# Kernel tuning notes

Hardware: AMD Instinct MI355X
Metric: run time of the kernel (lower is better)

Reference implementation:

```python
import jax, jax.numpy as jnp
import numpy as np

H = 768
NH = 12
HD = H // NH  # 64


def setup_inputs() -> dict:
    key = jax.random.key(0)
    ks = jax.random.split(key, 10)
    s = 0.02
    return {
        "hidden_states": jax.random.normal(ks[0], (2, 2048, H), dtype=jnp.float32),
        "attention_mask": jnp.ones((2, 2048), dtype=jnp.int32),
        "wq": jax.random.normal(ks[1], (H, H), dtype=jnp.float32) * s,
        "bq": jnp.zeros((H,), dtype=jnp.float32),
        "wk": jax.random.normal(ks[2], (H, H), dtype=jnp.float32) * s,
        "bk": jnp.zeros((H,), dtype=jnp.float32),
        "wv": jax.random.normal(ks[3], (H, H), dtype=jnp.float32) * s,
        "bv": jnp.zeros((H,), dtype=jnp.float32),
        "wo": jax.random.normal(ks[4], (H, H), dtype=jnp.float32) * s,
        "bo": jnp.zeros((H,), dtype=jnp.float32),
    }


def reference(hidden_states, attention_mask, wq, bq, wk, bk, wv, bv, wo, bo):
    b, s, h = hidden_states.shape
    # torch Linear: x @ W.T + b
    def proj(w, bias):
        y = jnp.einsum("bsh,oh->bso", hidden_states, w) + bias
        return y.reshape(b, s, NH, HD).transpose(0, 2, 1, 3)  # [b, nh, s, hd]

    q = proj(wq, bq)
    k = proj(wk, bk)
    v = proj(wv, bv)

    scores = jnp.einsum("bhqd,bhkd->bhqk", q, k) / jnp.sqrt(jnp.float32(HD))
    mask = attention_mask[:, None, None, :]  # [b,1,1,s]
    scores = jnp.where(mask == 0, jnp.float32(-1e9), scores)
    probs = jax.nn.softmax(scores, axis=-1)
    # dropout is identity in eval mode
    ctx = jnp.einsum("bhqk,bhkd->bhqd", probs, v)
    ctx = ctx.transpose(0, 2, 1, 3).reshape(b, s, h)
    return jnp.einsum("bsh,oh->bso", ctx, wo) + bo
```

## Files before the change

kernel.cpp:

```cpp
#include <hip/hip_runtime.h>

#define NH   12
#define HD   64
#define H    768
#define B_   2
#define S_   2048
#define MTOT (B_*S_)
#define SPLK 2

typedef short bf16x8 __attribute__((ext_vector_type(8)));
typedef float f32x4  __attribute__((ext_vector_type(4)));
typedef float f32x16 __attribute__((ext_vector_type(16)));
typedef unsigned uint32x2 __attribute__((ext_vector_type(2)));

#define MFMA16(a,b,c) __builtin_amdgcn_mfma_f32_16x16x32_bf16((a),(b),(c),0,0,0)
#define MFMA32(a,b,c) __builtin_amdgcn_mfma_f32_32x32x16_bf16((a),(b),(c),0,0,0)
#define GLL16(g,l) __builtin_amdgcn_global_load_lds( \
    (const __attribute__((address_space(1))) void*)(g), \
    (__attribute__((address_space(3))) void*)(l), 16, 0, 0)
#define EXP2F(x) __builtin_amdgcn_exp2f(x)
#define SCHEDB() __builtin_amdgcn_sched_barrier(0)
#define SBAR()   __builtin_amdgcn_s_barrier()

#if __has_builtin(__builtin_amdgcn_permlane32_swap)
__device__ __forceinline__ uint32x2 plswap(unsigned a, unsigned b){
    return __builtin_amdgcn_permlane32_swap(a, b, false, false);
}
#else
__device__ __forceinline__ uint32x2 plswap(unsigned a, unsigned b){
    const int hi = (threadIdx.x & 63) >> 5;
    const unsigned pa = (unsigned)__shfl_xor((int)a, 32);
    const unsigned pb = (unsigned)__shfl_xor((int)b, 32);
    uint32x2 r;
    r.x = hi ? pb : a;
    r.y = hi ? b  : pa;
    return r;
}
#endif

__device__ __forceinline__ float cross32_max(float x){
    uint32x2 r = plswap(__float_as_uint(x), __float_as_uint(x));
    return fmaxf(__uint_as_float(r.x), __uint_as_float(r.y));
}
__device__ __forceinline__ float cross32_add(float x){
    uint32x2 r = plswap(__float_as_uint(x), __float_as_uint(x));
    return __uint_as_float(r.x) + __uint_as_float(r.y);
}

__device__ __forceinline__ unsigned short f2bf(float x){
    union { float f; unsigned u; } c; c.f = x;
    unsigned r = (c.u + 0x7FFFu + ((c.u >> 16) & 1u)) >> 16;
    return (unsigned short)r;
}

#define XB 3072
#define WB 576
__global__ __launch_bounds__(256) void prep(
    const float* __restrict__ hs,
    const float* __restrict__ wq, const float* __restrict__ wk,
    const float* __restrict__ wv, const float* __restrict__ wo,
    unsigned short* __restrict__ Xh, unsigned short* __restrict__ Wqkv,
    unsigned short* __restrict__ Wo_)
{
    const int bid = blockIdx.x;
    const float* src;
    unsigned short* dst;
    int ib;
    if (bid < XB){
        src = hs; dst = Xh; ib = bid;
    } else {
        const int w = (bid - XB) / WB;
        ib = (bid - XB) - w*WB;
        src = (w==0)?wq:(w==1)?wk:(w==2)?wv:wo;
        dst = (w < 3) ? (Wqkv + (size_t)w*768*H) : Wo_;
    }
    const size_t i = (size_t)ib*256 + threadIdx.x;
    const float4 v = ((const float4*)src)[i];
    ushort4 o;
    o.x = f2bf(v.x); o.y = f2bf(v.y); o.z = f2bf(v.z); o.w = f2bf(v.w);
    ((ushort4*)dst)[i] = o;
}

template<int MODE>
__global__ __launch_bounds__(256) void gemm_bf16(
    const unsigned short* __restrict__ A, const unsigned short* __restrict__ Bm,
    const float* __restrict__ b0, const float* __restrict__ b1,
    const float* __restrict__ b2,
    float* __restrict__ out,
    unsigned short* __restrict__ Qh, unsigned short* __restrict__ Kh,
    unsigned short* __restrict__ Vh)
{
    constexpr int NIT = H/32;

    __shared__ unsigned short As[2][64*32];
    __shared__ unsigned short Bs[2][128*32];
    const int tid = threadIdx.x, lane = tid & 63, wave = tid >> 6;
    const int m0 = blockIdx.x*64, n0 = blockIdx.y*128;
    const int wr = wave >> 1, wc = wave & 1;
    const int frow = lane & 15, foct = lane >> 4;
    const int arow = lane >> 2;
    const int achk = ((lane & 3) ^ (arow & 3)) * 8;
    const int fswz = (foct ^ (frow & 3)) * 8;

    auto STAGE = [&](int bufi, int kp){
        {
            const int r0 = wave*16;
            GLL16(A + (size_t)(m0 + r0 + arow)*H + kp + achk, &As[bufi][r0*32]);
        }
        #pragma unroll
        for (int i = 0; i < 2; ++i){
            const int r0 = (wave*2 + i)*16;
            GLL16(Bm + (size_t)(n0 + r0 + arow)*H + kp + achk, &Bs[bufi][r0*32]);
        }
    };

    STAGE(0, 0);
    STAGE(1, 32);

    f32x4 acc[2][4] = {};

    for (int it = 0; it < NIT; ++it){
        const int cur = it & 1;
        if (it + 1 < NIT) asm volatile("s_waitcnt vmcnt(3)");
        else              asm volatile("s_waitcnt vmcnt(0)");
        SCHEDB();
        SBAR();
        SCHEDB();

        bf16x8 af[2], bfv[4];
        #pragma unroll
        for (int i = 0; i < 2; ++i)
            af[i]  = *(const bf16x8*)&As[cur][(wr*32 + 16*i + frow)*32 + fswz];
        #pragma unroll
        for (int j = 0; j < 4; ++j)
            bfv[j] = *(const bf16x8*)&Bs[cur][(wc*64 + 16*j + frow)*32 + fswz];
        #pragma unroll
        for (int i = 0; i < 2; ++i)
            #pragma unroll
            for (int j = 0; j < 4; ++j)
                acc[i][j] = MFMA16(af[i], bfv[j], acc[i][j]);

        SCHEDB();
        SBAR();
        SCHEDB();
        if (it + 2 < NIT) STAGE(cur, (it + 2)*32);
    }

    if (MODE == 0){
        #pragma unroll
        for (int i = 0; i < 2; ++i){
            const int m = m0 + wr*32 + 16*i + 4*foct;
            #pragma unroll
            for (int j = 0; j < 4; ++j){
                const int n = n0 + wc*64 + 16*j + frow;
                const float bb = b0[n];
                #pragma unroll
                for (int r = 0; r < 4; ++r)
                    out[(size_t)(m + r)*H + n] = acc[i][j][r] + bb;
            }
        }
    } else {
        const int sect = n0 / 768;
        const float* bias = (sect==0) ? b0 : (sect==1) ? b1 : b2;
        const float qs = (sect==0) ? 0.125f*1.44269504f : 1.0f;
        unsigned short* Ph = (sect==0) ? Qh : Kh;
        #pragma unroll
        for (int i = 0; i < 2; ++i){
            const int m  = m0 + wr*32 + 16*i + 4*foct;
            const int bb = m >> 11, ss = m & (S_-1);
            #pragma unroll
            for (int j = 0; j < 4; ++j){
                const int nn = (n0 - sect*768) + wc*64 + 16*j + frow;
                const float bv_ = bias[nn];
                const int hh = nn >> 6, dd = nn & 63;
                unsigned short hi[4];
                #pragma unroll
                for (int r = 0; r < 4; ++r)
                    hi[r] = f2bf((acc[i][j][r] + bv_) * qs);
                if (sect < 2){
                    const size_t basep = ((size_t)(bb*NH + hh)*S_)*HD + dd;
                    #pragma unroll
                    for (int r = 0; r < 4; ++r)
                        Ph[basep + (size_t)(ss + r)*HD] = hi[r];
                } else {
                    const size_t a = ((size_t)(bb*NH + hh)*HD + dd)*S_ + ss;
                    ushort4 ph; ph.x=hi[0]; ph.y=hi[1]; ph.z=hi[2]; ph.w=hi[3];
                    *(ushort4*)&Vh[a] = ph;
                }
            }
        }
    }
}

__global__ __launch_bounds__(256, 3) void attn_mfma(
    const unsigned short* __restrict__ Qh, const unsigned short* __restrict__ Kh,
    const unsigned short* __restrict__ Vh,
    const int* __restrict__ mask, float* __restrict__ Op, float* __restrict__ mlb)
{
    __shared__ unsigned short Ksh[2][64*64];
    __shared__ unsigned short Vsh[2][64*64];

    const int tid = threadIdx.x, lane = tid & 63, wave = tid >> 6;
    const int q0 = blockIdx.x*128, h = blockIdx.y;
    const int b = blockIdx.z & 1, part = blockIdx.z >> 1;
    const int l31 = lane & 31, hi = lane >> 5, l7 = lane & 7;
    const size_t base  = (size_t)(b*NH + h)*S_;
    const size_t vbase = (size_t)(b*NH + h)*HD;
    const int srow = lane >> 3;
    const int schk = ((lane & 7) ^ srow) * 8;
    const int NTH = 16;
    const int t0 = part*NTH;

    auto STAGE = [&](int bufi, int t){
        if (wave < 2){
            #pragma unroll
            for (int i = 0; i < 4; ++i){
                const int r0 = (wave*4 + i)*8, row = r0 + srow;
                GLL16(Kh + (base + (size_t)t*64 + row)*HD + schk, &Ksh[bufi][r0*64]);
            }
        } else {
            #pragma unroll
            for (int i = 0; i < 4; ++i){
                const int r0 = ((wave-2)*4 + i)*8, row = r0 + srow;
                GLL16(Vh + (vbase + row)*S_ + (size_t)t*64 + schk, &Vsh[bufi][r0*64]);
            }
        }
    };

    unsigned mbits = 0;
    {
        const int* mp = mask + (size_t)b*S_ + lane*32;
        #pragma unroll
        for (int j = 0; j < 32; ++j) mbits |= (mp[j] ? 1u : 0u) << j;
    }

    bf16x8 qf[4];
    {
        const size_t qr = (base + q0 + wave*32 + l31)*HD;
        #pragma unroll
        for (int ds = 0; ds < 4; ++ds)
            qf[ds] = *(const bf16x8*)&Qh[qr + ds*16 + hi*8];
    }

    STAGE(0, t0);
    STAGE(1, t0 + 1);

    float mR = -1e30f, lR = 0.f;
    f32x16 o0 = {}, o1 = {};

    for (int tt = 0; tt < NTH; ++tt){
        const int t = t0 + tt, cur = tt & 1;
        if (tt + 1 < NTH) asm volatile("s_waitcnt vmcnt(4)");
        else              asm volatile("s_waitcnt vmcnt(0)");
        SCHEDB();
        SBAR();
        SCHEDB();

        f32x16 s0 = {}, s1 = {};
        __builtin_amdgcn_s_setprio(1);
        #pragma unroll
        for (int ds = 0; ds < 4; ++ds){
            const int c0 = ((2*ds + hi) ^ l7)*8;
            const bf16x8 kh0 = *(const bf16x8*)&Ksh[cur][l31*64 + c0];
            const bf16x8 kh1 = *(const bf16x8*)&Ksh[cur][(32+l31)*64 + c0];
            s0 = MFMA32(kh0, qf[ds], s0);
            s1 = MFMA32(kh1, qf[ds], s1);
        }
        __builtin_amdgcn_s_setprio(0);

        {
            const unsigned bm_lo = (unsigned)__shfl((int)mbits, 2*t);
            const unsigned bm_hi = (unsigned)__shfl((int)mbits, 2*t + 1);
            const unsigned long long mb = ((unsigned long long)bm_hi << 32) | bm_lo;
            if (~mb){
                #pragma unroll
                for (int r = 0; r < 16; ++r){
                    const int key = (r&3) + 8*(r>>2) + 4*hi;
                    if (!((mb >> key) & 1))      s0[r] = -1e9f;
                    if (!((mb >> (key+32)) & 1)) s1[r] = -1e9f;
                }
            }
        }

        float vmax = -1e30f;
        #pragma unroll
        for (int r = 0; r < 16; ++r) vmax = fmaxf(vmax, fmaxf(s0[r], s1[r]));
        vmax = cross32_max(vmax);
        if (!__all(vmax <= mR + 11.5f)){
            const float mnew = fmaxf(mR, vmax);
            const float sc = EXP2F(mR - mnew);
            mR = mnew; lR *= sc;
            #pragma unroll
            for (int r = 0; r < 16; ++r){ o0[r] *= sc; o1[r] *= sc; }
        }
        float ps = 0.f;
        #pragma unroll
        for (int r = 0; r < 16; ++r){
            s0[r] = EXP2F(s0[r] - mR);
            s1[r] = EXP2F(s1[r] - mR);
            ps += s0[r] + s1[r];
        }
        ps = cross32_add(ps);
        lR += ps;

        bf16x8 pf[4];
        #pragma unroll
        for (int s = 0; s < 4; ++s){
            const f32x16& pv = (s < 2) ? s0 : s1;
            const int rb = (s & 1)*8;
            unsigned w0, w1, w2, w3;
            asm("v_cvt_pk_bf16_f32 %0, %1, %2" : "=v"(w0) : "v"(pv[rb+0]), "v"(pv[rb+1]));
            asm("v_cvt_pk_bf16_f32 %0, %1, %2" : "=v"(w1) : "v"(pv[rb+2]), "v"(pv[rb+3]));
            asm("v_cvt_pk_bf16_f32 %0, %1, %2" : "=v"(w2) : "v"(pv[rb+4]), "v"(pv[rb+5]));
            asm("v_cvt_pk_bf16_f32 %0, %1, %2" : "=v"(w3) : "v"(pv[rb+6]), "v"(pv[rb+7]));
            const uint32x2 r02 = plswap(w0, w2);
            const uint32x2 r13 = plswap(w1, w3);
            union { uint4 u; bf16x8 v; } pk;
            pk.u.x = r02.x; pk.u.y = r13.x; pk.u.z = r02.y; pk.u.w = r13.y;
            pf[s] = pk.v;
        }

        __builtin_amdgcn_s_setprio(1);
        #pragma unroll
        for (int s = 0; s < 4; ++s){
            const int c0 = ((2*s + hi) ^ l7)*8;
            const bf16x8 vh0 = *(const bf16x8*)&Vsh[cur][l31*64 + c0];
            const bf16x8 vh1 = *(const bf16x8*)&Vsh[cur][(32+l31)*64 + c0];
            o0 = MFMA32(vh0, pf[s], o0);
            o1 = MFMA32(vh1, pf[s], o1);
        }
        __builtin_amdgcn_s_setprio(0);

        SCHEDB();
        SBAR();
        SCHEDB();
        if (tt + 2 < NTH) STAGE(cur, t + 2);
    }

    const int qg = q0 + wave*32 + l31;
    const size_t NQ = (size_t)B_*NH*S_;
    const size_t gq = ((size_t)b*NH + h)*S_ + qg;
    float* Od = Op + (part*NQ + gq)*HD;
    #pragma unroll
    for (int a = 0; a < 4; ++a){
        const int d0 = 8*a + 4*hi;
        f32x4 v0, v1;
        #pragma unroll
        for (int r = 0; r < 4; ++r){ v0[r] = o0[a*4+r]; v1[r] = o1[a*4+r]; }
        *(f32x4*)&Od[d0]      = v0;
        *(f32x4*)&Od[32 + d0] = v1;
    }
    if (hi == 0){
        mlb[(part*NQ + gq)*2]     = mR;
        mlb[(part*NQ + gq)*2 + 1] = lR;
    }
}

__global__ __launch_bounds__(256) void attn_combine(
    const float* __restrict__ Op, const float* __restrict__ mlb,
    unsigned short* __restrict__ Cs)
{
    const int tid = threadIdx.x;
    const int gq = blockIdx.x*16 + (tid >> 4);
    const int dl = (tid & 15)*4;
    const int s = gq & (S_-1);
    const int bh = gq >> 11;
    const int h = bh % NH, b = bh / NH;
    const size_t NQ = (size_t)B_*NH*S_;

    float m_[SPLK], l_[SPLK];
    #pragma unroll
    for (int i = 0; i < SPLK; ++i){
        m_[i] = mlb[(i*NQ + gq)*2];
        l_[i] = mlb[(i*NQ + gq)*2 + 1];
    }
    float mm = m_[0];
    #pragma unroll
    for (int i = 1; i < SPLK; ++i) mm = fmaxf(mm, m_[i]);
    float w_[SPLK], den = 0.f;
    #pragma unroll
    for (int i = 0; i < SPLK; ++i){
        w_[i] = __builtin_amdgcn_exp2f(m_[i] - mm);
        den += l_[i]*w_[i];
    }
    const float inv = 1.0f / den;

    float v0 = 0.f, v1 = 0.f, v2 = 0.f, v3 = 0.f;
    #pragma unroll
    for (int i = 0; i < SPLK; ++i){
        const float4 O = *(const float4*)&Op[(i*NQ + gq)*HD + dl];
        v0 += O.x*w_[i]; v1 += O.y*w_[i]; v2 += O.z*w_[i]; v3 += O.w*w_[i];
    }
    v0 *= inv; v1 *= inv; v2 *= inv; v3 *= inv;

    ushort4 ph;
    ph.x = f2bf(v0); ph.y = f2bf(v1); ph.z = f2bf(v2); ph.w = f2bf(v3);
    *(ushort4*)&Cs[((size_t)b*S_ + s)*H + h*HD + dl] = ph;
}

extern "C" void kernel_launch(void* const* d_in, const int* in_sizes, int n_in,
                              void* d_out, int out_size, void* d_ws, size_t ws_size,
                              hipStream_t stream) {
    const float* hs = (const float*)d_in[0];
    const int*  msk = (const int*)  d_in[1];
    const float* wq = (const float*)d_in[2];
    const float* bq = (const float*)d_in[3];
    const float* wk = (const float*)d_in[4];
    const float* bk = (const float*)d_in[5];
    const float* wv = (const float*)d_in[6];
    const float* bv = (const float*)d_in[7];
    const float* wo = (const float*)d_in[8];
    const float* bo = (const float*)d_in[9];
    float* out = (float*)d_out;

    const size_t XH_E   = (size_t)MTOT*H;
    const size_t WQKV_E = (size_t)2304*H;
    const size_t WO_E   = (size_t)768*H;
    const size_t QKV_E  = (size_t)B_*NH*S_*HD;
    const size_t CS_E   = (size_t)MTOT*H;

    unsigned short* p = (unsigned short*)d_ws;
    unsigned short* Xh   = p; p += XH_E;
    unsigned short* Wqkv = p; p += WQKV_E;
    unsigned short* Wo_  = p; p += WO_E;
    unsigned short* Qh = p; p += QKV_E;
    unsigned short* Kh = p; p += QKV_E;
    unsigned short* Vh = p; p += QKV_E;
    unsigned short* Cs = p; p += CS_E;
    float* Op  = (float*)p;
    float* mlb = Op + (size_t)SPLK*QKV_E;

    prep<<<dim3(XB + 4*WB), 256, 0, stream>>>(
        hs, wq, wk, wv, wo, Xh, Wqkv, Wo_);
    gemm_bf16<1><<<dim3(MTOT/64, 2304/128), 256, 0, stream>>>(
        Xh, Wqkv, bq, bk, bv, nullptr, Qh, Kh, Vh);
    attn_mfma<<<dim3(S_/128, NH, B_*SPLK), 256, 0, stream>>>(
        Qh, Kh, Vh, msk, Op, mlb);
    attn_combine<<<dim3((B_*NH*S_)/16), 256, 0, stream>>>(Op, mlb, Cs);
    gemm_bf16<0><<<dim3(MTOT/64, H/128), 256, 0, stream>>>(
        Cs, Wo_, bo, nullptr, nullptr, out,
        nullptr, nullptr, nullptr);
}
```

Measured before the change: 107.5 us.

## Fuse split-K attention combine into attention kernel via intra-block key split

The two global key-split partitions move inside one block: waves 0-1 process even key tiles and waves 2-3 odd key tiles for the same 64 queries. The partial outputs are merged through LDS at the end, so the separate combine kernel and the fp32 partial O/m/l round trip through global memory go away. In exchange, staging loses its double-buffer prefetch overlap (each iteration waits on vmcnt(0) for the tile pair just loaded), and each block now covers 64 queries instead of 128, so K/V are reloaded more often per query.

```diff
diff --git a/kernel.cpp b/kernel.cpp
--- a/kernel.cpp
+++ b/kernel.cpp
@@ -6,7 +6,6 @@
 #define B_   2
 #define S_   2048
 #define MTOT (B_*S_)
-#define SPLK 2
 
 typedef short bf16x8 __attribute__((ext_vector_type(8)));
 typedef float f32x4  __attribute__((ext_vector_type(4)));
@@ -195,34 +194,44 @@
 __global__ __launch_bounds__(256, 3) void attn_mfma(
     const unsigned short* __restrict__ Qh, const unsigned short* __restrict__ Kh,
     const unsigned short* __restrict__ Vh,
-    const int* __restrict__ mask, float* __restrict__ Op, float* __restrict__ mlb)
+    const int* __restrict__ mask, unsigned short* __restrict__ Cs)
 {
     __shared__ unsigned short Ksh[2][64*64];
     __shared__ unsigned short Vsh[2][64*64];
 
     const int tid = threadIdx.x, lane = tid & 63, wave = tid >> 6;
-    const int q0 = blockIdx.x*128, h = blockIdx.y;
-    const int b = blockIdx.z & 1, part = blockIdx.z >> 1;
+    const int q0 = blockIdx.x*64, h = blockIdx.y, b = blockIdx.z;
+    const int qb = wave & 1, kp2 = wave >> 1;
     const int l31 = lane & 31, hi = lane >> 5, l7 = lane & 7;
     const size_t base  = (size_t)(b*NH + h)*S_;
     const size_t vbase = (size_t)(b*NH + h)*HD;
     const int srow = lane >> 3;
     const int schk = ((lane & 7) ^ srow) * 8;
-    const int NTH = 16;
-    const int t0 = part*NTH;
-
-    auto STAGE = [&](int bufi, int t){
-        if (wave < 2){
-            #pragma unroll
-            for (int i = 0; i < 4; ++i){
-                const int r0 = (wave*4 + i)*8, row = r0 + srow;
-                GLL16(Kh + (base + (size_t)t*64 + row)*HD + schk, &Ksh[bufi][r0*64]);
+
+    auto STAGE2 = [&](int te){
+        if (wave == 0){
+            #pragma unroll
+            for (int i = 0; i < 8; ++i){
+                const int r0 = i*8, row = r0 + srow;
+                GLL16(Kh + (base + (size_t)te*64 + row)*HD + schk, &Ksh[0][r0*64]);
+            }
+        } else if (wave == 1){
+            #pragma unroll
+            for (int i = 0; i < 8; ++i){
+                const int r0 = i*8, row = r0 + srow;
+                GLL16(Vh + (vbase + row)*S_ + (size_t)te*64 + schk, &Vsh[0][r0*64]);
+            }
+        } else if (wave == 2){
+            #pragma unroll
+            for (int i = 0; i < 8; ++i){
+                const int r0 = i*8, row = r0 + srow;
+                GLL16(Kh + (base + (size_t)(te+1)*64 + row)*HD + schk, &Ksh[1][r0*64]);
             }
         } else {
             #pragma unroll
-            for (int i = 0; i < 4; ++i){
-                const int r0 = ((wave-2)*4 + i)*8, row = r0 + srow;
-                GLL16(Vh + (vbase + row)*S_ + (size_t)t*64 + schk, &Vsh[bufi][r0*64]);
+            for (int i = 0; i < 8; ++i){
+                const int r0 = i*8, row = r0 + srow;
+                GLL16(Vh + (vbase + row)*S_ + (size_t)(te+1)*64 + schk, &Vsh[1][r0*64]);
             }
         }
     };
@@ -236,22 +245,20 @@
 
     bf16x8 qf[4];
     {
-        const size_t qr = (base + q0 + wave*32 + l31)*HD;
+        const size_t qr = (base + q0 + qb*32 + l31)*HD;
         #pragma unroll
         for (int ds = 0; ds < 4; ++ds)
             qf[ds] = *(const bf16x8*)&Qh[qr + ds*16 + hi*8];
     }
 
-    STAGE(0, t0);
-    STAGE(1, t0 + 1);
+    STAGE2(0);
 
     float mR = -1e30f, lR = 0.f;
     f32x16 o0 = {}, o1 = {};
 
-    for (int tt = 0; tt < NTH; ++tt){
-        const int t = t0 + tt, cur = tt & 1;
-        if (tt + 1 < NTH) asm volatile("s_waitcnt vmcnt(4)");
-        else              asm volatile("s_waitcnt vmcnt(0)");
+    for (int tt = 0; tt < 16; ++tt){
+        const int t = 2*tt + kp2;
+        asm volatile("s_waitcnt vmcnt(0)");
         SCHEDB();
         SBAR();
         SCHEDB();
@@ -261,8 +268,8 @@
         #pragma unroll
         for (int ds = 0; ds < 4; ++ds){
             const int c0 = ((2*ds + hi) ^ l7)*8;
-            const bf16x8 kh0 = *(const bf16x8*)&Ksh[cur][l31*64 + c0];
-            const bf16x8 kh1 = *(const bf16x8*)&Ksh[cur][(32+l31)*64 + c0];
+            const bf16x8 kh0 = *(const bf16x8*)&Ksh[kp2][l31*64 + c0];
+            const bf16x8 kh1 = *(const bf16x8*)&Ksh[kp2][(32+l31)*64 + c0];
             s0 = MFMA32(kh0, qf[ds], s0);
             s1 = MFMA32(kh1, qf[ds], s1);
         }
@@ -324,8 +331,8 @@
         #pragma unroll
         for (int s = 0; s < 4; ++s){
             const int c0 = ((2*s + hi) ^ l7)*8;
-            const bf16x8 vh0 = *(const bf16x8*)&Vsh[cur][l31*64 + c0];
-            const bf16x8 vh1 = *(const bf16x8*)&Vsh[cur][(32+l31)*64 + c0];
+            const bf16x8 vh0 = *(const bf16x8*)&Vsh[kp2][l31*64 + c0];
+            const bf16x8 vh1 = *(const bf16x8*)&Vsh[kp2][(32+l31)*64 + c0];
             o0 = MFMA32(vh0, pf[s], o0);
             o1 = MFMA32(vh1, pf[s], o1);
         }
@@ -334,68 +341,52 @@
         SCHEDB();
         SBAR();
         SCHEDB();
-        if (tt + 2 < NTH) STAGE(cur, t + 2);
-    }
-
-    const int qg = q0 + wave*32 + l31;
-    const size_t NQ = (size_t)B_*NH*S_;
-    const size_t gq = ((size_t)b*NH + h)*S_ + qg;
-    float* Od = Op + (part*NQ + gq)*HD;
-    #pragma unroll
-    for (int a = 0; a < 4; ++a){
-        const int d0 = 8*a + 4*hi;
-        f32x4 v0, v1;
-        #pragma unroll
-        for (int r = 0; r < 4; ++r){ v0[r] = o0[a*4+r]; v1[r] = o1[a*4+r]; }
-        *(f32x4*)&Od[d0]      = v0;
-        *(f32x4*)&Od[32 + d0] = v1;
-    }
-    if (hi == 0){
-        mlb[(part*NQ + gq)*2]     = mR;
-        mlb[(part*NQ + gq)*2 + 1] = lR;
-    }
-}
-
-__global__ __launch_bounds__(256) void attn_combine(
-    const float* __restrict__ Op, const float* __restrict__ mlb,
-    unsigned short* __restrict__ Cs)
-{
-    const int tid = threadIdx.x;
-    const int gq = blockIdx.x*16 + (tid >> 4);
-    const int dl = (tid & 15)*4;
-    const int s = gq & (S_-1);
-    const int bh = gq >> 11;
-    const int h = bh % NH, b = bh / NH;
-    const size_t NQ = (size_t)B_*NH*S_;
-
-    float m_[SPLK], l_[SPLK];
-    #pragma unroll
-    for (int i = 0; i < SPLK; ++i){
-        m_[i] = mlb[(i*NQ + gq)*2];
-        l_[i] = mlb[(i*NQ + gq)*2 + 1];
-    }
-    float mm = m_[0];
-    #pragma unroll
-    for (int i = 1; i < SPLK; ++i) mm = fmaxf(mm, m_[i]);
-    float w_[SPLK], den = 0.f;
-    #pragma unroll
-    for (int i = 0; i < SPLK; ++i){
-        w_[i] = __builtin_amdgcn_exp2f(m_[i] - mm);
-        den += l_[i]*w_[i];
-    }
-    const float inv = 1.0f / den;
-
-    float v0 = 0.f, v1 = 0.f, v2 = 0.f, v3 = 0.f;
-    #pragma unroll
-    for (int i = 0; i < SPLK; ++i){
-        const float4 O = *(const float4*)&Op[(i*NQ + gq)*HD + dl];
-        v0 += O.x*w_[i]; v1 += O.y*w_[i]; v2 += O.z*w_[i]; v3 += O.w*w_[i];
-    }
-    v0 *= inv; v1 *= inv; v2 *= inv; v3 *= inv;
-
-    ushort4 ph;
-    ph.x = f2bf(v0); ph.y = f2bf(v1); ph.z = f2bf(v2); ph.w = f2bf(v3);
-    *(ushort4*)&Cs[((size_t)b*S_ + s)*H + h*HD + dl] = ph;
+        if (tt + 1 < 16) STAGE2(2*(tt + 1));
+    }
+
+    float* Olds = (float*)&Ksh[0][0];
+    float* Mlds = (float*)&Vsh[0][0];
+    const int qi = qb*32 + l31;
+
+    if (kp2 == 1){
+        #pragma unroll
+        for (int a = 0; a < 4; ++a){
+            const int d0 = 8*a + 4*hi;
+            f32x4 v0, v1;
+            #pragma unroll
+            for (int r = 0; r < 4; ++r){ v0[r] = o0[a*4+r]; v1[r] = o1[a*4+r]; }
+            *(f32x4*)&Olds[qi*64 + d0]      = v0;
+            *(f32x4*)&Olds[qi*64 + 32 + d0] = v1;
+        }
+        if (hi == 0){
+            Mlds[qi*2]     = mR;
+            Mlds[qi*2 + 1] = lR;
+        }
+    }
+    __syncthreads();
+
+    if (kp2 == 0){
+        const float mo = Mlds[qi*2], lo = Mlds[qi*2 + 1];
+        const float mm = fmaxf(mR, mo);
+        const float we = EXP2F(mR - mm), wo_ = EXP2F(mo - mm);
+        const float inv = 1.0f / (lR*we + lo*wo_);
+        const int sg = q0 + qi;
+        unsigned short* Crow = Cs + ((size_t)b*S_ + sg)*H + h*HD;
+        #pragma unroll
+        for (int a = 0; a < 4; ++a){
+            const int d0 = 8*a + 4*hi;
+            ushort4 u0, u1;
+            #pragma unroll
+            for (int r = 0; r < 4; ++r){
+                const float e0 = (o0[a*4+r]*we + Olds[qi*64 + d0 + r]*wo_)*inv;
+                const float e1 = (o1[a*4+r]*we + Olds[qi*64 + 32 + d0 + r]*wo_)*inv;
+                ((unsigned short*)&u0)[r] = f2bf(e0);
+                ((unsigned short*)&u1)[r] = f2bf(e1);
+            }
+            *(ushort4*)&Crow[d0]      = u0;
+            *(ushort4*)&Crow[32 + d0] = u1;
+        }
+    }
 }
 
 extern "C" void kernel_launch(void* const* d_in, const int* in_sizes, int n_in,
@@ -427,16 +418,13 @@
     unsigned short* Kh = p; p += QKV_E;
     unsigned short* Vh = p; p += QKV_E;
     unsigned short* Cs = p; p += CS_E;
-    float* Op  = (float*)p;
-    float* mlb = Op + (size_t)SPLK*QKV_E;
 
     prep<<<dim3(XB + 4*WB), 256, 0, stream>>>(
         hs, wq, wk, wv, wo, Xh, Wqkv, Wo_);
     gemm_bf16<1><<<dim3(MTOT/64, 2304/128), 256, 0, stream>>>(
         Xh, Wqkv, bq, bk, bv, nullptr, Qh, Kh, Vh);
-    attn_mfma<<<dim3(S_/128, NH, B_*SPLK), 256, 0, stream>>>(
-        Qh, Kh, Vh, msk, Op, mlb);
-    attn_combine<<<dim3((B_*NH*S_)/16), 256, 0, stream>>>(Op, mlb, Cs);
+    attn_mfma<<<dim3(S_/64, NH, B_), 256, 0, stream>>>(
+        Qh, Kh, Vh, msk, Cs);
     gemm_bf16<0><<<dim3(MTOT/64, H/128), 256, 0, stream>>>(
         Cs, Wo_, bo, nullptr, nullptr, out,
         nullptr, nullptr, nullptr);
```

Result: faster. 101.7 us (-5.4%).
